# Optimization experiments

Measured on AMD Instinct MI355X. Metric: run time of the kernel, lower is better.

## Reference

```python
import jax, jax.numpy as jnp
import numpy as np

B, T, C = 2, 2048, 1024
NH = 16
HD = C // NH

def setup_inputs() -> dict:
    key = jax.random.key(0)
    ks = jax.random.split(key, 5)
    s = 0.02
    return {
        "x": jax.random.normal(ks[0], (B, T, C), dtype=jnp.float32),
        "W_qkv": jax.random.normal(ks[1], (C, 3 * C), dtype=jnp.float32) * s,
        "b_qkv": jnp.zeros((3 * C,), dtype=jnp.float32),
        "W_proj": jax.random.normal(ks[2], (C, C), dtype=jnp.float32) * s,
        "b_proj": jnp.zeros((C,), dtype=jnp.float32),
    }

def reference(x, W_qkv, b_qkv, W_proj, b_proj):
    Bx, Tx, Cx = x.shape
    qkv = x @ W_qkv + b_qkv                      # [B,T,3C]
    q, k, v = jnp.split(qkv, 3, axis=-1)
    # [B,T,C] -> [B,NH,T,HD]
    def heads(t):
        return t.reshape(Bx, Tx, NH, HD).transpose(0, 2, 1, 3)
    q, k, v = heads(q), heads(k), heads(v)
    scores = jnp.einsum("bhqd,bhkd->bhqk", q, k) / jnp.sqrt(jnp.float32(HD))
    causal = jnp.tril(jnp.ones((Tx, Tx), dtype=bool))
    scores = jnp.where(causal[None, None, :, :], scores, jnp.float32(-jnp.inf))
    attn = jax.nn.softmax(scores, axis=-1)       # dropout p=0 (eval)
    out = jnp.einsum("bhqk,bhkd->bhqd", attn, v)
    out = out.transpose(0, 2, 1, 3).reshape(Bx, Tx, Cx)
    return out @ W_proj + b_proj
```

## Files before the change

### kernel.cpp

```cpp
#include <hip/hip_runtime.h>
#include <math.h>

#define B_  2
#define T_  2048
#define C_  1024
#define NH_ 16
#define HD_ 64

typedef _Float16 half8  __attribute__((ext_vector_type(8)));
typedef _Float16 half4v __attribute__((ext_vector_type(4)));
typedef float    f32x4  __attribute__((ext_vector_type(4)));

__device__ __forceinline__ unsigned short f2h(float f) {
    _Float16 h = (_Float16)f;
    return __builtin_bit_cast(unsigned short, h);
}

__device__ __forceinline__ void gload_lds16(const void* g, void* l) {
    __builtin_amdgcn_global_load_lds(
        (const __attribute__((address_space(1))) unsigned int*)g,
        (__attribute__((address_space(3))) unsigned int*)l, 16, 0, 0);
}

__global__ __launch_bounds__(256)
void convert_x(const float* __restrict__ x, _Float16* __restrict__ xh, int n8)
{
    const int i = blockIdx.x * 256 + threadIdx.x;
    if (i < n8) {
        const float4 a = reinterpret_cast<const float4*>(x)[2 * i];
        const float4 b = reinterpret_cast<const float4*>(x)[2 * i + 1];
        half8 o;
        o[0] = (_Float16)a.x; o[1] = (_Float16)a.y;
        o[2] = (_Float16)a.z; o[3] = (_Float16)a.w;
        o[4] = (_Float16)b.x; o[5] = (_Float16)b.y;
        o[6] = (_Float16)b.z; o[7] = (_Float16)b.w;
        *reinterpret_cast<half8*>(&xh[(size_t)i * 8]) = o;
    }
}

__global__ __launch_bounds__(256)
void convert_wt(const float* __restrict__ W, _Float16* __restrict__ Wt,
                int K, int N)
{
    __shared__ float t[64][65];
    const int tid = threadIdx.x;
    const int n0 = blockIdx.x * 64, k0 = blockIdx.y * 64;

    for (int i = tid; i < 64 * 16; i += 256) {
        const int r = i >> 4, c4 = (i & 15) * 4;
        const float4 v = *reinterpret_cast<const float4*>(
            &W[(size_t)(k0 + r) * N + n0 + c4]);
        t[r][c4 + 0] = v.x; t[r][c4 + 1] = v.y;
        t[r][c4 + 2] = v.z; t[r][c4 + 3] = v.w;
    }
    __syncthreads();
    for (int i = tid; i < 64 * 16; i += 256) {
        const int r = i >> 4, c4 = (i & 15) * 4;
        half4v o;
        o[0] = (_Float16)t[c4 + 0][r];
        o[1] = (_Float16)t[c4 + 1][r];
        o[2] = (_Float16)t[c4 + 2][r];
        o[3] = (_Float16)t[c4 + 3][r];
        *reinterpret_cast<half4v*>(&Wt[(size_t)(n0 + r) * K + k0 + c4]) = o;
    }
}

template<bool QKV_SCATTER>
__global__ __launch_bounds__(256)
void gemm_mfma(const _Float16* __restrict__ A, const _Float16* __restrict__ Bt,
               const float* __restrict__ bias, float* __restrict__ Cout,
               int M, int N, int K,
               _Float16* __restrict__ qh, _Float16* __restrict__ kh,
               _Float16* __restrict__ vh)
{
    __shared__ __align__(16) _Float16 Asl[2][128 * 32];
    __shared__ __align__(16) _Float16 Bsl[2][128 * 32];

    const int tid  = threadIdx.x;
    const int w    = tid >> 6;
    const int lane = tid & 63;
    const int c    = lane & 15;
    const int g    = lane >> 4;
    const int wr   = w >> 1, wc = w & 1;
    const int bm   = blockIdx.y * 128, bn = blockIdx.x * 128;

    f32x4 acc[4][4] = {};

    auto stage = [&](int buf, int k0) {
        #pragma unroll
        for (int it = 0; it < 2; ++it) {
            const int e   = it * 256 + tid;
            const int row = e & 127, kc = e >> 7;
            const char* ldsA = (const char*)&Asl[buf][0];
            const char* ldsB = (const char*)&Bsl[buf][0];
            const int dst = (it * 256 + (tid & ~63)) * 16;
            gload_lds16(A  + (size_t)(bm + row) * K + k0 + kc * 8, (void*)(ldsA + dst));
            gload_lds16(Bt + (size_t)(bn + row) * K + k0 + kc * 8, (void*)(ldsB + dst));
        }
    };

    stage(0, 0);
    __syncthreads();

    for (int k0 = 0, it = 0; k0 < K; k0 += 32, ++it) {
        const int cur = it & 1;
        if (k0 + 32 < K) stage(cur ^ 1, k0 + 32);

        half8 af[4], bf[4];
        #pragma unroll
        for (int i = 0; i < 4; ++i) {
            const int row = wr * 64 + i * 16 + c;
            af[i] = *reinterpret_cast<const half8*>(
                (const char*)&Asl[cur][0] + (g * 128 + row) * 16);
        }
        #pragma unroll
        for (int j = 0; j < 4; ++j) {
            const int row = wc * 64 + j * 16 + c;
            bf[j] = *reinterpret_cast<const half8*>(
                (const char*)&Bsl[cur][0] + (g * 128 + row) * 16);
        }
        #pragma unroll
        for (int i = 0; i < 4; ++i)
            #pragma unroll
            for (int j = 0; j < 4; ++j)
                acc[i][j] = __builtin_amdgcn_mfma_f32_16x16x32_f16(
                    af[i], bf[j], acc[i][j], 0, 0, 0);

        __syncthreads();
    }

    #pragma unroll
    for (int i = 0; i < 4; ++i) {
        const int row0 = bm + wr * 64 + i * 16 + g * 4;
        #pragma unroll
        for (int j = 0; j < 4; ++j) {
            const int col = bn + wc * 64 + j * 16 + c;
            const float bv = bias[col];
            #pragma unroll
            for (int r2 = 0; r2 < 4; ++r2) {
                const float v = acc[i][j][r2] + bv;
                const int rr = row0 + r2;
                if (QKV_SCATTER) {
                    const int which = col >> 10;
                    const int cc = col & 1023;
                    const int hh = cc >> 6;
                    const int d  = cc & 63;
                    const int bb = rr >> 11;
                    const int t  = rr & 2047;
                    const size_t bhh = (size_t)(bb * NH_ + hh);
                    if (which == 0)
                        qh[(bhh * T_ + t) * HD_ + d] = (_Float16)(v * 0.125f);
                    else if (which == 1)
                        kh[(bhh * T_ + t) * HD_ + d] = (_Float16)v;
                    else
                        vh[(bhh * HD_ + d) * T_ + t] = (_Float16)v;
                } else {
                    Cout[(size_t)rr * N + col] = v;
                }
            }
        }
    }
}

__global__ __launch_bounds__(256)
void attn_kernel(const _Float16* __restrict__ Q,
                 const _Float16* __restrict__ K,
                 const _Float16* __restrict__ Vt,
                 _Float16* __restrict__ Out)
{
    __shared__ __align__(16) unsigned char Qs[8192];
    __shared__ __align__(16) unsigned char Ks[2][8192];
    __shared__ __align__(16) unsigned char Vs[2][8192];
    __shared__ __align__(16) unsigned char Ps[4][2048];

    const int tid  = threadIdx.x;
    const int w    = tid >> 6;
    const int lane = tid & 63;
    const int c    = lane & 15;
    const int g    = lane >> 4;
    const int qt   = (T_ / 64 - 1) - blockIdx.x;
    const int h    = blockIdx.y;
    const int b    = blockIdx.z;

    const size_t bh = (size_t)(b * NH_ + h) * T_ * HD_;
    const _Float16* Qg = Q + bh;
    const _Float16* Kg = K + bh;
    const _Float16* Vg = Vt + bh;

    auto stage_kv = [&](int buf, int kt) {
        #pragma unroll
        for (int it = 0; it < 2; ++it) {
            const int chunk = it * 256 + tid;
            const int row = chunk >> 3, s = chunk & 7;
            const int ss = s ^ (row & 7);
            gload_lds16(Kg + (size_t)(kt * 64 + row) * HD_ + ss * 8,
                        (char*)Ks[buf] + it * 4096 + (tid & ~63) * 16);
            gload_lds16(Vg + (size_t)row * T_ + kt * 64 + ss * 8,
                        (char*)Vs[buf] + it * 4096 + (tid & ~63) * 16);
        }
    };

    auto ldfrag = [&](const unsigned char* base, int row, int slot) -> half8 {
        return *reinterpret_cast<const half8*>(
            base + row * 128 + ((slot ^ (row & 7)) * 16));
    };

    #pragma unroll
    for (int it = 0; it < 2; ++it) {
        const int chunk = it * 256 + tid;
        const int row = chunk >> 3, s = chunk & 7;
        const int ss = s ^ (row & 7);
        gload_lds16(Qg + (size_t)(qt * 64 + row) * HD_ + ss * 8,
                    (char*)Qs + it * 4096 + (tid & ~63) * 16);
    }
    stage_kv(0, 0);
    __syncthreads();

    float mcol = -1e30f, lcol = 0.f;
    f32x4 Oacc[4] = {};

    for (int kt = 0; kt <= qt; ++kt) {
        const int cur = kt & 1;
        if (kt < qt) stage_kv(cur ^ 1, kt + 1);

        half8 qf[2];
        #pragma unroll
        for (int ks = 0; ks < 2; ++ks)
            qf[ks] = ldfrag(Qs, w * 16 + c, ks * 4 + g);

        f32x4 Sacc[4] = {};
        #pragma unroll
        for (int t = 0; t < 4; ++t)
            #pragma unroll
            for (int ks = 0; ks < 2; ++ks) {
                const half8 kf = ldfrag(Ks[cur], t * 16 + c, ks * 4 + g);
                Sacc[t] = __builtin_amdgcn_mfma_f32_16x16x32_f16(
                    kf, qf[ks], Sacc[t], 0, 0, 0);
            }

        if (kt == qt) {
            const int q_l = w * 16 + c;
            #pragma unroll
            for (int t = 0; t < 4; ++t)
                #pragma unroll
                for (int r2 = 0; r2 < 4; ++r2)
                    if (t * 16 + g * 4 + r2 > q_l) Sacc[t][r2] = -1e30f;
        }

        float tmax = -1e30f;
        #pragma unroll
        for (int t = 0; t < 4; ++t)
            #pragma unroll
            for (int r2 = 0; r2 < 4; ++r2) tmax = fmaxf(tmax, Sacc[t][r2]);
        tmax = fmaxf(tmax, __shfl_xor(tmax, 16));
        tmax = fmaxf(tmax, __shfl_xor(tmax, 32));
        const float mnew  = fmaxf(mcol, tmax);
        const float alpha = __expf(mcol - mnew);
        mcol = mnew;

        float psum = 0.f;
        unsigned pk[4][2];
        #pragma unroll
        for (int t = 0; t < 4; ++t) {
            const float p0 = __expf(Sacc[t][0] - mnew);
            const float p1 = __expf(Sacc[t][1] - mnew);
            const float p2 = __expf(Sacc[t][2] - mnew);
            const float p3 = __expf(Sacc[t][3] - mnew);
            psum += (p0 + p1) + (p2 + p3);
            pk[t][0] = (unsigned)f2h(p0) | ((unsigned)f2h(p1) << 16);
            pk[t][1] = (unsigned)f2h(p2) | ((unsigned)f2h(p3) << 16);
        }
        psum += __shfl_xor(psum, 16);
        psum += __shfl_xor(psum, 32);
        lcol = lcol * alpha + psum;

        {
            unsigned char* pbase = Ps[w];
            #pragma unroll
            for (int t = 0; t < 4; ++t)
                #pragma unroll
                for (int rp = 0; rp < 2; ++rp) {
                    const int off = (32 * t + 8 * g + 4 * rp) ^ ((c & 7) << 4);
                    *reinterpret_cast<unsigned*>(pbase + c * 128 + off) = pk[t][rp];
                }
        }

        #pragma unroll
        for (int r2 = 0; r2 < 4; ++r2) {
            const float av = __shfl(alpha, g * 20 + r2);
            #pragma unroll
            for (int dt = 0; dt < 4; ++dt) Oacc[dt][r2] *= av;
        }

        asm volatile("s_waitcnt lgkmcnt(0)" ::: "memory");
        __builtin_amdgcn_sched_barrier(0);

        half8 pf[2];
        #pragma unroll
        for (int ks = 0; ks < 2; ++ks)
            pf[ks] = ldfrag(Ps[w], c, ks * 4 + g);
        #pragma unroll
        for (int dt = 0; dt < 4; ++dt)
            #pragma unroll
            for (int ks = 0; ks < 2; ++ks) {
                const half8 vf = ldfrag(Vs[cur], dt * 16 + c, ks * 4 + g);
                Oacc[dt] = __builtin_amdgcn_mfma_f32_16x16x32_f16(
                    pf[ks], vf, Oacc[dt], 0, 0, 0);
            }

        __syncthreads();
    }

    const float invl = 1.0f / lcol;
    #pragma unroll
    for (int r2 = 0; r2 < 4; ++r2) {
        const float il = __shfl(invl, g * 20 + r2);
        const int qgl = qt * 64 + w * 16 + g * 4 + r2;
        _Float16* orow = Out + (size_t)(b * T_ + qgl) * C_ + h * HD_;
        #pragma unroll
        for (int dt = 0; dt < 4; ++dt)
            orow[dt * 16 + c] = (_Float16)(Oacc[dt][r2] * il);
    }
}

extern "C" void kernel_launch(void* const* d_in, const int* in_sizes, int n_in,
                              void* d_out, int out_size, void* d_ws, size_t ws_size,
                              hipStream_t stream) {
    const float* x      = (const float*)d_in[0];
    const float* W_qkv  = (const float*)d_in[1];
    const float* b_qkv  = (const float*)d_in[2];
    const float* W_proj = (const float*)d_in[3];
    const float* b_proj = (const float*)d_in[4];
    float* out = (float*)d_out;

    const size_t M4 = (size_t)B_ * T_ * C_;
    _Float16* xh  = (_Float16*)d_ws;
    _Float16* wqt = xh  + M4;
    _Float16* wpt = wqt + 3 * C_ * C_;
    _Float16* qh  = wpt + (size_t)C_ * C_;
    _Float16* kh  = qh  + M4;
    _Float16* vh  = kh  + M4;
    _Float16* ah  = vh  + M4;

    const dim3 blk(256);

    convert_x<<<dim3((B_ * T_ * C_ / 8 + 255) / 256), blk, 0, stream>>>(
        x, xh, B_ * T_ * C_ / 8);
    convert_wt<<<dim3(3 * C_ / 64, C_ / 64), blk, 0, stream>>>(
        W_qkv, wqt, C_, 3 * C_);
    convert_wt<<<dim3(C_ / 64, C_ / 64), blk, 0, stream>>>(
        W_proj, wpt, C_, C_);

    gemm_mfma<true><<<dim3(3 * C_ / 128, B_ * T_ / 128), blk, 0, stream>>>(
        xh, wqt, b_qkv, nullptr, B_ * T_, 3 * C_, C_, qh, kh, vh);

    attn_kernel<<<dim3(T_ / 64, NH_, B_), blk, 0, stream>>>(qh, kh, vh, ah);

    gemm_mfma<false><<<dim3(C_ / 128, B_ * T_ / 128), blk, 0, stream>>>(
        ah, wpt, b_proj, out, B_ * T_, C_, C_, nullptr, nullptr, nullptr);
}
```

Measured before the change: 277.4 us.

## Pair complementary causal query tiles per attention block for load balance and K/V reuse

Each attention block now processes two query tiles, p and its mirror T/64-1-p, so every block does the same amount of causal work. Each K/V tile is staged once and reused for both query tiles, and the grid shrinks to half as many blocks. In exchange the block needs more LDS and more registers for the two accumulator sets, which may lower occupancy. With fewer blocks, 512 across the chip, latency is also less well hidden.

```diff
diff --git a/kernel.cpp b/kernel.cpp
--- a/kernel.cpp
+++ b/kernel.cpp
@@ -168,17 +168,20 @@
                  const _Float16* __restrict__ Vt,
                  _Float16* __restrict__ Out)
 {
-    __shared__ __align__(16) unsigned char Qs[8192];
+    __shared__ __align__(16) unsigned char Qs[16384];
     __shared__ __align__(16) unsigned char Ks[2][8192];
     __shared__ __align__(16) unsigned char Vs[2][8192];
-    __shared__ __align__(16) unsigned char Ps[4][2048];
+    __shared__ __align__(16) unsigned char Psa[4][2048];
+    __shared__ __align__(16) unsigned char Psb[4][2048];
 
     const int tid  = threadIdx.x;
     const int w    = tid >> 6;
     const int lane = tid & 63;
     const int c    = lane & 15;
     const int g    = lane >> 4;
-    const int qt   = (T_ / 64 - 1) - blockIdx.x;
+    const int p    = blockIdx.x;
+    const int qa   = p;
+    const int qb   = (T_ / 64 - 1) - p;
     const int h    = blockIdx.y;
     const int b    = blockIdx.z;
 
@@ -206,120 +209,212 @@
     };
 
     #pragma unroll
-    for (int it = 0; it < 2; ++it) {
+    for (int it = 0; it < 4; ++it) {
         const int chunk = it * 256 + tid;
         const int row = chunk >> 3, s = chunk & 7;
         const int ss = s ^ (row & 7);
-        gload_lds16(Qg + (size_t)(qt * 64 + row) * HD_ + ss * 8,
+        const int qrow = (row < 64) ? (qa * 64 + row) : (qb * 64 + row - 64);
+        gload_lds16(Qg + (size_t)qrow * HD_ + ss * 8,
                     (char*)Qs + it * 4096 + (tid & ~63) * 16);
     }
     stage_kv(0, 0);
     __syncthreads();
 
-    float mcol = -1e30f, lcol = 0.f;
-    f32x4 Oacc[4] = {};
-
-    for (int kt = 0; kt <= qt; ++kt) {
+    half8 qfa[2], qfb[2];
+    #pragma unroll
+    for (int ks = 0; ks < 2; ++ks) {
+        qfa[ks] = ldfrag(Qs, w * 16 + c, ks * 4 + g);
+        qfb[ks] = ldfrag(Qs + 8192, w * 16 + c, ks * 4 + g);
+    }
+
+    float ma = -1e30f, la = 0.f, mb = -1e30f, lb = 0.f;
+    f32x4 Oa[4] = {}, Ob[4] = {};
+
+    for (int kt = 0; kt <= qb; ++kt) {
         const int cur = kt & 1;
-        if (kt < qt) stage_kv(cur ^ 1, kt + 1);
-
-        half8 qf[2];
-        #pragma unroll
-        for (int ks = 0; ks < 2; ++ks)
-            qf[ks] = ldfrag(Qs, w * 16 + c, ks * 4 + g);
-
-        f32x4 Sacc[4] = {};
+        if (kt < qb) stage_kv(cur ^ 1, kt + 1);
+        const bool doA = (kt <= qa);
+
+        f32x4 Sb[4] = {};
         #pragma unroll
         for (int t = 0; t < 4; ++t)
             #pragma unroll
             for (int ks = 0; ks < 2; ++ks) {
                 const half8 kf = ldfrag(Ks[cur], t * 16 + c, ks * 4 + g);
-                Sacc[t] = __builtin_amdgcn_mfma_f32_16x16x32_f16(
-                    kf, qf[ks], Sacc[t], 0, 0, 0);
+                Sb[t] = __builtin_amdgcn_mfma_f32_16x16x32_f16(
+                    kf, qfb[ks], Sb[t], 0, 0, 0);
             }
-
-        if (kt == qt) {
+        f32x4 Sa[4] = {};
+        if (doA) {
+            #pragma unroll
+            for (int t = 0; t < 4; ++t)
+                #pragma unroll
+                for (int ks = 0; ks < 2; ++ks) {
+                    const half8 kf = ldfrag(Ks[cur], t * 16 + c, ks * 4 + g);
+                    Sa[t] = __builtin_amdgcn_mfma_f32_16x16x32_f16(
+                        kf, qfa[ks], Sa[t], 0, 0, 0);
+                }
+        }
+
+        if (kt == qb) {
             const int q_l = w * 16 + c;
             #pragma unroll
             for (int t = 0; t < 4; ++t)
                 #pragma unroll
                 for (int r2 = 0; r2 < 4; ++r2)
-                    if (t * 16 + g * 4 + r2 > q_l) Sacc[t][r2] = -1e30f;
-        }
-
-        float tmax = -1e30f;
+                    if (t * 16 + g * 4 + r2 > q_l) Sb[t][r2] = -1e30f;
+        }
+        if (doA && kt == qa) {
+            const int q_l = w * 16 + c;
+            #pragma unroll
+            for (int t = 0; t < 4; ++t)
+                #pragma unroll
+                for (int r2 = 0; r2 < 4; ++r2)
+                    if (t * 16 + g * 4 + r2 > q_l) Sa[t][r2] = -1e30f;
+        }
+
+        float tb = -1e30f;
         #pragma unroll
         for (int t = 0; t < 4; ++t)
             #pragma unroll
-            for (int r2 = 0; r2 < 4; ++r2) tmax = fmaxf(tmax, Sacc[t][r2]);
-        tmax = fmaxf(tmax, __shfl_xor(tmax, 16));
-        tmax = fmaxf(tmax, __shfl_xor(tmax, 32));
-        const float mnew  = fmaxf(mcol, tmax);
-        const float alpha = __expf(mcol - mnew);
-        mcol = mnew;
-
-        float psum = 0.f;
-        unsigned pk[4][2];
+            for (int r2 = 0; r2 < 4; ++r2) tb = fmaxf(tb, Sb[t][r2]);
+        tb = fmaxf(tb, __shfl_xor(tb, 16));
+        tb = fmaxf(tb, __shfl_xor(tb, 32));
+        const float mnb = fmaxf(mb, tb);
+        const float alb = __expf(mb - mnb);
+        mb = mnb;
+        float psb = 0.f;
+        unsigned pkb[4][2];
         #pragma unroll
         for (int t = 0; t < 4; ++t) {
-            const float p0 = __expf(Sacc[t][0] - mnew);
-            const float p1 = __expf(Sacc[t][1] - mnew);
-            const float p2 = __expf(Sacc[t][2] - mnew);
-            const float p3 = __expf(Sacc[t][3] - mnew);
-            psum += (p0 + p1) + (p2 + p3);
-            pk[t][0] = (unsigned)f2h(p0) | ((unsigned)f2h(p1) << 16);
-            pk[t][1] = (unsigned)f2h(p2) | ((unsigned)f2h(p3) << 16);
-        }
-        psum += __shfl_xor(psum, 16);
-        psum += __shfl_xor(psum, 32);
-        lcol = lcol * alpha + psum;
-
+            const float p0 = __expf(Sb[t][0] - mnb);
+            const float p1 = __expf(Sb[t][1] - mnb);
+            const float p2 = __expf(Sb[t][2] - mnb);
+            const float p3 = __expf(Sb[t][3] - mnb);
+            psb += (p0 + p1) + (p2 + p3);
+            pkb[t][0] = (unsigned)f2h(p0) | ((unsigned)f2h(p1) << 16);
+            pkb[t][1] = (unsigned)f2h(p2) | ((unsigned)f2h(p3) << 16);
+        }
+        psb += __shfl_xor(psb, 16);
+        psb += __shfl_xor(psb, 32);
+        lb = lb * alb + psb;
         {
-            unsigned char* pbase = Ps[w];
+            unsigned char* pb = Psb[w];
             #pragma unroll
             for (int t = 0; t < 4; ++t)
                 #pragma unroll
                 for (int rp = 0; rp < 2; ++rp) {
                     const int off = (32 * t + 8 * g + 4 * rp) ^ ((c & 7) << 4);
-                    *reinterpret_cast<unsigned*>(pbase + c * 128 + off) = pk[t][rp];
-                }
-        }
-
+                    *reinterpret_cast<unsigned*>(pb + c * 128 + off) = pkb[t][rp];
+                }
+        }
         #pragma unroll
         for (int r2 = 0; r2 < 4; ++r2) {
-            const float av = __shfl(alpha, g * 20 + r2);
-            #pragma unroll
-            for (int dt = 0; dt < 4; ++dt) Oacc[dt][r2] *= av;
+            const float av = __shfl(alb, g * 20 + r2);
+            #pragma unroll
+            for (int dt = 0; dt < 4; ++dt) Ob[dt][r2] *= av;
+        }
+
+        if (doA) {
+            float ta = -1e30f;
+            #pragma unroll
+            for (int t = 0; t < 4; ++t)
+                #pragma unroll
+                for (int r2 = 0; r2 < 4; ++r2) ta = fmaxf(ta, Sa[t][r2]);
+            ta = fmaxf(ta, __shfl_xor(ta, 16));
+            ta = fmaxf(ta, __shfl_xor(ta, 32));
+            const float mna = fmaxf(ma, ta);
+            const float ala = __expf(ma - mna);
+            ma = mna;
+            float psa = 0.f;
+            unsigned pka[4][2];
+            #pragma unroll
+            for (int t = 0; t < 4; ++t) {
+                const float p0 = __expf(Sa[t][0] - mna);
+                const float p1 = __expf(Sa[t][1] - mna);
+                const float p2 = __expf(Sa[t][2] - mna);
+                const float p3 = __expf(Sa[t][3] - mna);
+                psa += (p0 + p1) + (p2 + p3);
+                pka[t][0] = (unsigned)f2h(p0) | ((unsigned)f2h(p1) << 16);
+                pka[t][1] = (unsigned)f2h(p2) | ((unsigned)f2h(p3) << 16);
+            }
+            psa += __shfl_xor(psa, 16);
+            psa += __shfl_xor(psa, 32);
+            la = la * ala + psa;
+            unsigned char* pa = Psa[w];
+            #pragma unroll
+            for (int t = 0; t < 4; ++t)
+                #pragma unroll
+                for (int rp = 0; rp < 2; ++rp) {
+                    const int off = (32 * t + 8 * g + 4 * rp) ^ ((c & 7) << 4);
+                    *reinterpret_cast<unsigned*>(pa + c * 128 + off) = pka[t][rp];
+                }
+            #pragma unroll
+            for (int r2 = 0; r2 < 4; ++r2) {
+                const float av = __shfl(ala, g * 20 + r2);
+                #pragma unroll
+                for (int dt = 0; dt < 4; ++dt) Oa[dt][r2] *= av;
+            }
         }
 
         asm volatile("s_waitcnt lgkmcnt(0)" ::: "memory");
         __builtin_amdgcn_sched_barrier(0);
 
-        half8 pf[2];
-        #pragma unroll
-        for (int ks = 0; ks < 2; ++ks)
-            pf[ks] = ldfrag(Ps[w], c, ks * 4 + g);
-        #pragma unroll
-        for (int dt = 0; dt < 4; ++dt)
-            #pragma unroll
-            for (int ks = 0; ks < 2; ++ks) {
-                const half8 vf = ldfrag(Vs[cur], dt * 16 + c, ks * 4 + g);
-                Oacc[dt] = __builtin_amdgcn_mfma_f32_16x16x32_f16(
-                    pf[ks], vf, Oacc[dt], 0, 0, 0);
-            }
+        {
+            half8 pf[2];
+            #pragma unroll
+            for (int ks = 0; ks < 2; ++ks)
+                pf[ks] = ldfrag(Psb[w], c, ks * 4 + g);
+            #pragma unroll
+            for (int dt = 0; dt < 4; ++dt)
+                #pragma unroll
+                for (int ks = 0; ks < 2; ++ks) {
+                    const half8 vf = ldfrag(Vs[cur], dt * 16 + c, ks * 4 + g);
+                    Ob[dt] = __builtin_amdgcn_mfma_f32_16x16x32_f16(
+                        pf[ks], vf, Ob[dt], 0, 0, 0);
+                }
+        }
+        if (doA) {
+            half8 pf[2];
+            #pragma unroll
+            for (int ks = 0; ks < 2; ++ks)
+                pf[ks] = ldfrag(Psa[w], c, ks * 4 + g);
+            #pragma unroll
+            for (int dt = 0; dt < 4; ++dt)
+                #pragma unroll
+                for (int ks = 0; ks < 2; ++ks) {
+                    const half8 vf = ldfrag(Vs[cur], dt * 16 + c, ks * 4 + g);
+                    Oa[dt] = __builtin_amdgcn_mfma_f32_16x16x32_f16(
+                        pf[ks], vf, Oa[dt], 0, 0, 0);
+                }
+        }
 
         __syncthreads();
     }
 
-    const float invl = 1.0f / lcol;
-    #pragma unroll
-    for (int r2 = 0; r2 < 4; ++r2) {
-        const float il = __shfl(invl, g * 20 + r2);
-        const int qgl = qt * 64 + w * 16 + g * 4 + r2;
-        _Float16* orow = Out + (size_t)(b * T_ + qgl) * C_ + h * HD_;
-        #pragma unroll
-        for (int dt = 0; dt < 4; ++dt)
-            orow[dt * 16 + c] = (_Float16)(Oacc[dt][r2] * il);
+    {
+        const float il0 = 1.0f / lb;
+        #pragma unroll
+        for (int r2 = 0; r2 < 4; ++r2) {
+            const float il = __shfl(il0, g * 20 + r2);
+            const int qgl = qb * 64 + w * 16 + g * 4 + r2;
+            _Float16* orow = Out + (size_t)(b * T_ + qgl) * C_ + h * HD_;
+            #pragma unroll
+            for (int dt = 0; dt < 4; ++dt)
+                orow[dt * 16 + c] = (_Float16)(Ob[dt][r2] * il);
+        }
+    }
+    {
+        const float il0 = 1.0f / la;
+        #pragma unroll
+        for (int r2 = 0; r2 < 4; ++r2) {
+            const float il = __shfl(il0, g * 20 + r2);
+            const int qgl = qa * 64 + w * 16 + g * 4 + r2;
+            _Float16* orow = Out + (size_t)(b * T_ + qgl) * C_ + h * HD_;
+            #pragma unroll
+            for (int dt = 0; dt < 4; ++dt)
+                orow[dt * 16 + c] = (_Float16)(Oa[dt][r2] * il);
+        }
     }
 }
 
@@ -354,7 +449,7 @@
     gemm_mfma<true><<<dim3(3 * C_ / 128, B_ * T_ / 128), blk, 0, stream>>>(
         xh, wqt, b_qkv, nullptr, B_ * T_, 3 * C_, C_, qh, kh, vh);
 
-    attn_kernel<<<dim3(T_ / 64, NH_, B_), blk, 0, stream>>>(qh, kh, vh, ah);
+    attn_kernel<<<dim3(T_ / 128, NH_, B_), blk, 0, stream>>>(qh, kh, vh, ah);
 
     gemm_mfma<false><<<dim3(C_ / 128, B_ * T_ / 128), blk, 0, stream>>>(
         ah, wpt, b_proj, out, B_ * T_, C_, C_, nullptr, nullptr, nullptr);
```

Result: faster. 239.5 us (-13.6%).
